# Kernel optimization log

Hardware: AMD Instinct MI355X
Metric: run time of the kernel (lower is better)

## Reference

```python
import jax, jax.numpy as jnp
import numpy as np

N_DRUGS = 4096
W_DIM = 512
N_SUB = 10
N_EDGES = 131072


def setup_inputs() -> dict:
    key = jax.random.key(0)
    k1, k2, k3, k4 = jax.random.split(key, 4)
    z_drug = jax.random.normal(k1, (N_DRUGS, W_DIM), dtype=jnp.float32)
    # glorot-ish init for weights
    global_weight = jax.random.normal(k2, (W_DIM, W_DIM), dtype=jnp.float32) * (2.0 / (2 * W_DIM)) ** 0.5
    local_diag = jax.random.normal(k3, (N_SUB, W_DIM), dtype=jnp.float32) * (2.0 / (W_DIM + 1)) ** 0.5
    batch_edges = jax.random.randint(k4, (2, N_EDGES), 0, N_DRUGS, dtype=jnp.int64)
    return {
        "z_drug": z_drug,
        "global_weight": global_weight,
        "local_diag": local_diag,
        "batch_edges": batch_edges,
        "edge_sub_type_idx": 2,
    }


def reference(z_drug, global_weight, local_diag, batch_edges, edge_sub_type_idx):
    # edge_type == 'drug_drug': z1 = z2 = z_drug
    row_embed = z_drug[batch_edges[0]]            # [B, D]
    col_embed = z_drug[batch_edges[1]]            # [B, D]
    d = local_diag[edge_sub_type_idx]             # [D] diagonal of local weight matrix
    # row @ diag(d) @ W @ diag(d) == ((row * d) @ W) * d
    p = ((row_embed * d) @ global_weight) * d     # [B, D]
    # diagonal(p @ col^T) == rowwise dot product
    score = jnp.sum(p * col_embed, axis=-1)       # [B]
    return jax.nn.sigmoid(score)
```

## Files before the change

### kernel.cpp

```cpp
#include <hip/hip_runtime.h>
#include <cstdint>

#define ND 4096
#define D  512

typedef __bf16 bf16x8 __attribute__((ext_vector_type(8)));
typedef float floatx4 __attribute__((ext_vector_type(4)));
typedef unsigned short ushort8 __attribute__((ext_vector_type(8)));

__device__ __forceinline__ float bf2f(unsigned short b) {
    return __uint_as_float(((unsigned int)b) << 16);
}
__device__ __forceinline__ unsigned short f2bf(float f) {
    unsigned int u = __float_as_uint(f);
    u += 0x7fffu + ((u >> 16) & 1u);
    return (unsigned short)(u >> 16);
}
__device__ __forceinline__ float lo16(unsigned int u) { return __uint_as_float(u << 16); }
__device__ __forceinline__ float hi16(unsigned int u) { return __uint_as_float(u & 0xffff0000u); }

__device__ __forceinline__ void gll16(const void* g, void* l) {
    __builtin_amdgcn_global_load_lds((const __attribute__((address_space(1))) unsigned int*)g,
                                     (__attribute__((address_space(3))) unsigned int*)l,
                                     16, 0, 0);
}

union U8B8 { ushort8 u; bf16x8 b; };

__device__ __forceinline__ int2 detect_flags(const unsigned short* z, const int* ed) {
    int lane = threadIdx.x & 63;
    unsigned short u = z[lane];
    int e = (u >> 7) & 0xFF;
    unsigned long long b0 = __ballot(e >= 96 && e <= 160);
    unsigned long long b1 = __ballot(ed[2 * lane + 1] == 0);
    int2 f;
    f.x = (__popcll(b0) >= 56) ? 1 : 0;
    f.y = (__popcll(b1) >= 56) ? 1 : 0;
    return f;
}

__global__ __launch_bounds__(256) void make_mt(const void* __restrict__ Wv,
                                               const void* __restrict__ ldv,
                                               const int* __restrict__ sub,
                                               unsigned short* __restrict__ Mt,
                                               const unsigned short* __restrict__ zdet,
                                               const int* __restrict__ eddet) {
    __shared__ float lds[64][65];
    int2 f = detect_flags(zdet, eddet);
    int bf = f.x;
    int su = sub[0];
    if ((unsigned)su > 9u) su = 2;
    int k0 = blockIdx.x * 64, n0 = blockIdx.y * 64;
    int j = threadIdx.x & 63;
    int w = threadIdx.x >> 6;

#pragma unroll
    for (int r = 0; r < 16; r++) {
        int k = k0 + w * 16 + r;
        float v = bf ? bf2f(((const unsigned short*)Wv)[k * D + n0 + j])
                     : ((const float*)Wv)[k * D + n0 + j];
        lds[w * 16 + r][j] = v;
    }
    __syncthreads();

    int k = k0 + j;
    float dk = bf ? bf2f(((const unsigned short*)ldv)[su * D + k])
                  : ((const float*)ldv)[su * D + k];
#pragma unroll
    for (int r = 0; r < 16; r++) {
        int n = n0 + w * 16 + r;
        float dn = bf ? bf2f(((const unsigned short*)ldv)[su * D + n])
                      : ((const float*)ldv)[su * D + n];
        Mt[n * D + k] = f2bf(lds[j][w * 16 + r] * dk * dn);
    }
}

template <bool BF>
__device__ void gemm_body(const void* __restrict__ z,
                          const unsigned short* __restrict__ Mt,
                          unsigned short* __restrict__ Y) {
    __shared__ __bf16 As[8 * 512];
    __shared__ __bf16 Bs[8 * 512];
    int tid = threadIdx.x;
    int w = tid >> 6, lane = tid & 63;
    int rl = lane & 15, quad = lane >> 4;
    int tm = blockIdx.x * 64, tn = blockIdx.y * 64;
    int wm = (w >> 1) * 32, wn = (w & 1) * 32;

    floatx4 acc[2][2] = {};
    for (int kk = 0; kk < D; kk += 64) {
        __syncthreads();
#pragma unroll
        for (int t = 0; t < 2; t++) {
            int kb = w * 2 + t;
            gll16(Mt + (tn + lane) * D + kk + kb * 8, Bs + kb * 512);
            if constexpr (BF) {
                gll16((const __bf16*)z + (tm + lane) * D + kk + kb * 8, As + kb * 512);
            } else {
                const float* zf = (const float*)z + (tm + lane) * D + kk + kb * 8;
                float4 f0 = *(const float4*)zf;
                float4 f1 = *(const float4*)(zf + 4);
                U8B8 cv;
                cv.u[0] = f2bf(f0.x); cv.u[1] = f2bf(f0.y); cv.u[2] = f2bf(f0.z); cv.u[3] = f2bf(f0.w);
                cv.u[4] = f2bf(f1.x); cv.u[5] = f2bf(f1.y); cv.u[6] = f2bf(f1.z); cv.u[7] = f2bf(f1.w);
                *(bf16x8*)(As + kb * 512 + lane * 8) = cv.b;
            }
        }
        __syncthreads();
#pragma unroll
        for (int kc = 0; kc < 64; kc += 32) {
            int kb0 = kc >> 3;
            bf16x8 a0 = *(const bf16x8*)(As + (kb0 + quad) * 512 + (wm + rl) * 8);
            bf16x8 a1 = *(const bf16x8*)(As + (kb0 + quad) * 512 + (wm + 16 + rl) * 8);
            bf16x8 b0 = *(const bf16x8*)(Bs + (kb0 + quad) * 512 + (wn + rl) * 8);
            bf16x8 b1 = *(const bf16x8*)(Bs + (kb0 + quad) * 512 + (wn + 16 + rl) * 8);
            acc[0][0] = __builtin_amdgcn_mfma_f32_16x16x32_bf16(a0, b0, acc[0][0], 0, 0, 0);
            acc[0][1] = __builtin_amdgcn_mfma_f32_16x16x32_bf16(a0, b1, acc[0][1], 0, 0, 0);
            acc[1][0] = __builtin_amdgcn_mfma_f32_16x16x32_bf16(a1, b0, acc[1][0], 0, 0, 0);
            acc[1][1] = __builtin_amdgcn_mfma_f32_16x16x32_bf16(a1, b1, acc[1][1], 0, 0, 0);
        }
    }
#pragma unroll
    for (int j = 0; j < 2; j++) {
        int col = tn + wn + j * 16 + rl;
#pragma unroll
        for (int i = 0; i < 2; i++) {
            int rbase = tm + wm + i * 16 + quad * 4;
#pragma unroll
            for (int r = 0; r < 4; r++)
                Y[(rbase + r) * D + col] = f2bf(acc[i][j][r]);
        }
    }
}

__global__ __launch_bounds__(256) void gemm_kernel(const void* __restrict__ z,
                                                   const unsigned short* __restrict__ Mt,
                                                   unsigned short* __restrict__ Y,
                                                   const int* __restrict__ eddet) {
    int2 f = detect_flags((const unsigned short*)z, eddet);
    if (f.x) gemm_body<true>(z, Mt, Y);
    else     gemm_body<false>(z, Mt, Y);
}

template <bool BF, bool I64>
__device__ void edge_body(const unsigned short* __restrict__ Y,
                          const void* __restrict__ z,
                          const int* __restrict__ ed,
                          float* __restrict__ partial,
                          void* __restrict__ out,
                          int E, int pass) {
    int gid = blockIdx.x * 256 + threadIdx.x;
    int lane = threadIdx.x & 63;
    int e = (gid >> 6) * 4 + (lane >> 4);
    int l = lane & 15;
    if (e >= E) return;
    int r, c;
    if constexpr (I64) { r = ed[2 * e]; c = ed[2 * (E + e)]; }
    else               { r = ed[e];     c = ed[E + e]; }
    r &= ND - 1; c &= ND - 1;

    int col = pass * 128 + l * 8;
    uint4 yu = *(const uint4*)(Y + r * D + col);
    float y0 = lo16(yu.x), y1 = hi16(yu.x), y2 = lo16(yu.y), y3 = hi16(yu.y);
    float y4 = lo16(yu.z), y5 = hi16(yu.z), y6 = lo16(yu.w), y7 = hi16(yu.w);
    float s;
    if constexpr (BF) {
        uint4 zu = *(const uint4*)((const unsigned short*)z + c * D + col);
        s  = y0 * lo16(zu.x) + y1 * hi16(zu.x);
        s += y2 * lo16(zu.y) + y3 * hi16(zu.y);
        s += y4 * lo16(zu.z) + y5 * hi16(zu.z);
        s += y6 * lo16(zu.w) + y7 * hi16(zu.w);
    } else {
        const float* zf = (const float*)z + c * D + col;
        float4 f0 = *(const float4*)zf;
        float4 f1 = *(const float4*)(zf + 4);
        s  = y0 * f0.x + y1 * f0.y + y2 * f0.z + y3 * f0.w;
        s += y4 * f1.x + y5 * f1.y + y6 * f1.z + y7 * f1.w;
    }
#pragma unroll
    for (int off = 8; off; off >>= 1)
        s += __shfl_xor(s, off, 64);

    if (l == 0) {
        if (pass == 0)      partial[e] = s;
        else if (pass < 3)  partial[e] += s;
        else {
            float t = s + partial[e];
            if (!(t > -1e30f && t < 1e30f)) t = 0.0f;
            float sig = 1.0f / (1.0f + __expf(-t));
            if constexpr (BF) ((unsigned short*)out)[e] = f2bf(sig);
            else              ((float*)out)[e] = sig;
        }
    }
}

__global__ __launch_bounds__(256) void edge_kernel(const unsigned short* __restrict__ Y,
                                                   const void* __restrict__ z,
                                                   const int* __restrict__ ed,
                                                   float* __restrict__ partial,
                                                   void* __restrict__ out,
                                                   int E, int pass) {
    int2 f = detect_flags((const unsigned short*)z, ed);
    if (f.x) { if (f.y) edge_body<true, true>(Y, z, ed, partial, out, E, pass);
               else     edge_body<true, false>(Y, z, ed, partial, out, E, pass); }
    else     { if (f.y) edge_body<false, true>(Y, z, ed, partial, out, E, pass);
               else     edge_body<false, false>(Y, z, ed, partial, out, E, pass); }
}

extern "C" void kernel_launch(void* const* d_in, const int* in_sizes, int n_in,
                              void* d_out, int out_size, void* d_ws, size_t ws_size,
                              hipStream_t stream) {
    const void* z     = d_in[0];
    const void* W     = d_in[1];
    const void* ldiag = d_in[2];
    const int* edges  = (const int*)d_in[3];
    const int* sub    = (const int*)d_in[4];
    int E = out_size;

    char* ws = (char*)d_ws;
    unsigned short* Y  = (unsigned short*)ws;
    unsigned short* Mt = (unsigned short*)(ws + 4194304);
    float* partial     = (float*)(ws + 4194304 + 524288);

    make_mt<<<dim3(D / 64, D / 64), 256, 0, stream>>>(W, ldiag, sub, Mt,
                                                      (const unsigned short*)z, edges);
    gemm_kernel<<<dim3(ND / 64, D / 64), 256, 0, stream>>>(z, Mt, Y, edges);
    int eblocks = (E + 15) / 16;
    for (int p = 0; p < 4; p++)
        edge_kernel<<<eblocks, 256, 0, stream>>>(Y, z, edges, partial, d_out, E, p);
}
```

Baseline: 126.7 us.

## Fuse all stages into one cooperative persistent kernel with grid syncs

Replaces the six separate launches (transform, GEMM, four edge passes) with a single cooperative kernel of 512 blocks that runs transform, GEMM and two column-half edge passes separated by grid-wide syncs. The edge stage is restructured so each wave loads 64 edge indices once and shuffles them out, processing 256 columns per pass with 32-lane reductions, and keeps partial sums in LDS instead of global memory. This aims to remove launch gaps and redundant index loads, in exchange for grid-sync overhead and a residency requirement. A fallback multi-kernel path is used if the cooperative launch fails.

```diff
diff --git a/kernel.cpp b/kernel.cpp
--- a/kernel.cpp
+++ b/kernel.cpp
@@ -1,8 +1,12 @@
 #include <hip/hip_runtime.h>
+#include <hip/hip_cooperative_groups.h>
 #include <cstdint>
+
+namespace cg = cooperative_groups;
 
 #define ND 4096
 #define D  512
+#define NBLK 512
 
 typedef __bf16 bf16x8 __attribute__((ext_vector_type(8)));
 typedef float floatx4 __attribute__((ext_vector_type(4)));
@@ -39,30 +43,21 @@
     return f;
 }
 
-__global__ __launch_bounds__(256) void make_mt(const void* __restrict__ Wv,
-                                               const void* __restrict__ ldv,
-                                               const int* __restrict__ sub,
-                                               unsigned short* __restrict__ Mt,
-                                               const unsigned short* __restrict__ zdet,
-                                               const int* __restrict__ eddet) {
-    __shared__ float lds[64][65];
-    int2 f = detect_flags(zdet, eddet);
-    int bf = f.x;
+__device__ void make_mt_body(const void* __restrict__ Wv, const void* __restrict__ ldv,
+                             const int* __restrict__ sub, int bf,
+                             unsigned short* __restrict__ Mt, int b, float (*xp)[65]) {
     int su = sub[0];
     if ((unsigned)su > 9u) su = 2;
-    int k0 = blockIdx.x * 64, n0 = blockIdx.y * 64;
-    int j = threadIdx.x & 63;
-    int w = threadIdx.x >> 6;
-
+    int k0 = (b & 7) * 64, n0 = (b >> 3) * 64;
+    int j = threadIdx.x & 63, w = threadIdx.x >> 6;
 #pragma unroll
     for (int r = 0; r < 16; r++) {
         int k = k0 + w * 16 + r;
         float v = bf ? bf2f(((const unsigned short*)Wv)[k * D + n0 + j])
                      : ((const float*)Wv)[k * D + n0 + j];
-        lds[w * 16 + r][j] = v;
+        xp[w * 16 + r][j] = v;
     }
     __syncthreads();
-
     int k = k0 + j;
     float dk = bf ? bf2f(((const unsigned short*)ldv)[su * D + k])
                   : ((const float*)ldv)[su * D + k];
@@ -71,20 +66,18 @@
         int n = n0 + w * 16 + r;
         float dn = bf ? bf2f(((const unsigned short*)ldv)[su * D + n])
                       : ((const float*)ldv)[su * D + n];
-        Mt[n * D + k] = f2bf(lds[j][w * 16 + r] * dk * dn);
+        Mt[n * D + k] = f2bf(xp[j][w * 16 + r] * dk * dn);
     }
 }
 
 template <bool BF>
-__device__ void gemm_body(const void* __restrict__ z,
-                          const unsigned short* __restrict__ Mt,
-                          unsigned short* __restrict__ Y) {
-    __shared__ __bf16 As[8 * 512];
-    __shared__ __bf16 Bs[8 * 512];
+__device__ void gemm_body(const void* __restrict__ z, const unsigned short* __restrict__ Mt,
+                          unsigned short* __restrict__ Y, int b,
+                          __bf16* As, __bf16* Bs) {
     int tid = threadIdx.x;
     int w = tid >> 6, lane = tid & 63;
     int rl = lane & 15, quad = lane >> 4;
-    int tm = blockIdx.x * 64, tn = blockIdx.y * 64;
+    int tm = (b >> 3) * 64, tn = (b & 7) * 64;
     int wm = (w >> 1) * 32, wn = (w & 1) * 32;
 
     floatx4 acc[2][2] = {};
@@ -133,78 +126,122 @@
     }
 }
 
-__global__ __launch_bounds__(256) void gemm_kernel(const void* __restrict__ z,
-                                                   const unsigned short* __restrict__ Mt,
-                                                   unsigned short* __restrict__ Y,
-                                                   const int* __restrict__ eddet) {
+template <bool BF, bool I64>
+__device__ void edge_half(const unsigned short* __restrict__ Y, const void* __restrict__ z,
+                          const int* __restrict__ ed, void* __restrict__ out,
+                          int E, int half, float* pbuf, int pbase) {
+    int lane = threadIdx.x & 63;
+    int w = threadIdx.x >> 6;
+    int wid = blockIdx.x * 4 + w;
+    int base = wid * 64;
+    int le = base + lane;
+    int r_l = 0, c_l = 0;
+    if (le < E) {
+        if constexpr (I64) { r_l = ed[2 * le]; c_l = ed[2 * (E + le)]; }
+        else               { r_l = ed[le];     c_l = ed[E + le]; }
+    }
+    r_l &= ND - 1; c_l &= ND - 1;
+    int g = lane >> 5;
+    int l = lane & 31;
+    int colbase = half * 256 + l * 8;
+
+#pragma unroll 4
+    for (int i = 0; i < 32; i++) {
+        int sube = i * 2 + g;
+        int r = __shfl(r_l, sube, 64);
+        int c = __shfl(c_l, sube, 64);
+        uint4 yu = *(const uint4*)(Y + r * D + colbase);
+        float y0 = lo16(yu.x), y1 = hi16(yu.x), y2 = lo16(yu.y), y3 = hi16(yu.y);
+        float y4 = lo16(yu.z), y5 = hi16(yu.z), y6 = lo16(yu.w), y7 = hi16(yu.w);
+        float s;
+        if constexpr (BF) {
+            uint4 zu = *(const uint4*)((const unsigned short*)z + c * D + colbase);
+            s  = y0 * lo16(zu.x) + y1 * hi16(zu.x);
+            s += y2 * lo16(zu.y) + y3 * hi16(zu.y);
+            s += y4 * lo16(zu.z) + y5 * hi16(zu.z);
+            s += y6 * lo16(zu.w) + y7 * hi16(zu.w);
+        } else {
+            const float* zf = (const float*)z + c * D + colbase;
+            float4 f0 = *(const float4*)zf;
+            float4 f1 = *(const float4*)(zf + 4);
+            s  = y0 * f0.x + y1 * f0.y + y2 * f0.z + y3 * f0.w;
+            s += y4 * f1.x + y5 * f1.y + y6 * f1.z + y7 * f1.w;
+        }
+#pragma unroll
+        for (int off = 16; off; off >>= 1)
+            s += __shfl_xor(s, off, 64);
+
+        if (l == 0 && base + sube < E) {
+            if (half == 0) {
+                pbuf[pbase + sube] = s;
+            } else {
+                float t = s + pbuf[pbase + sube];
+                if (!(t > -1e30f && t < 1e30f)) t = 0.0f;
+                float sig = 1.0f / (1.0f + __expf(-t));
+                if constexpr (BF) ((unsigned short*)out)[base + sube] = f2bf(sig);
+                else              ((float*)out)[base + sube] = sig;
+            }
+        }
+    }
+}
+
+__global__ __launch_bounds__(256, 2) void mega(const void* z, const void* Wv, const void* ldv,
+                                               const int* ed, const int* sub, void* out, int E,
+                                               unsigned short* Mt, unsigned short* Y) {
+    __shared__ float xp[64][65];
+    __shared__ __bf16 As[8 * 512];
+    __shared__ __bf16 Bs[8 * 512];
+    __shared__ float pls[256];
+    cg::grid_group grid = cg::this_grid();
+    int b = blockIdx.x;
+    int2 f = detect_flags((const unsigned short*)z, ed);
+
+    if (b < 64) make_mt_body(Wv, ldv, sub, f.x, Mt, b, xp);
+    __threadfence();
+    grid.sync();
+
+    if (f.x) gemm_body<true>(z, Mt, Y, b, As, Bs);
+    else     gemm_body<false>(z, Mt, Y, b, As, Bs);
+    __threadfence();
+    grid.sync();
+
+    int pbase = (threadIdx.x >> 6) * 64;
+    if (f.x) { if (f.y) edge_half<true, true >(Y, z, ed, out, E, 0, pls, pbase);
+               else     edge_half<true, false>(Y, z, ed, out, E, 0, pls, pbase); }
+    else     { if (f.y) edge_half<false, true >(Y, z, ed, out, E, 0, pls, pbase);
+               else     edge_half<false, false>(Y, z, ed, out, E, 0, pls, pbase); }
+    __threadfence();
+    grid.sync();
+
+    if (f.x) { if (f.y) edge_half<true, true >(Y, z, ed, out, E, 1, pls, pbase);
+               else     edge_half<true, false>(Y, z, ed, out, E, 1, pls, pbase); }
+    else     { if (f.y) edge_half<false, true >(Y, z, ed, out, E, 1, pls, pbase);
+               else     edge_half<false, false>(Y, z, ed, out, E, 1, pls, pbase); }
+}
+
+__global__ __launch_bounds__(256) void fb_make_mt(const void* Wv, const void* ldv,
+                                                  const int* sub, unsigned short* Mt,
+                                                  const unsigned short* zdet, const int* eddet) {
+    __shared__ float xp[64][65];
+    int2 f = detect_flags(zdet, eddet);
+    make_mt_body(Wv, ldv, sub, f.x, Mt, blockIdx.x, xp);
+}
+__global__ __launch_bounds__(256) void fb_gemm(const void* z, const unsigned short* Mt,
+                                               unsigned short* Y, const int* eddet) {
+    __shared__ __bf16 As[8 * 512], Bs[8 * 512];
     int2 f = detect_flags((const unsigned short*)z, eddet);
-    if (f.x) gemm_body<true>(z, Mt, Y);
-    else     gemm_body<false>(z, Mt, Y);
-}
-
-template <bool BF, bool I64>
-__device__ void edge_body(const unsigned short* __restrict__ Y,
-                          const void* __restrict__ z,
-                          const int* __restrict__ ed,
-                          float* __restrict__ partial,
-                          void* __restrict__ out,
-                          int E, int pass) {
-    int gid = blockIdx.x * 256 + threadIdx.x;
-    int lane = threadIdx.x & 63;
-    int e = (gid >> 6) * 4 + (lane >> 4);
-    int l = lane & 15;
-    if (e >= E) return;
-    int r, c;
-    if constexpr (I64) { r = ed[2 * e]; c = ed[2 * (E + e)]; }
-    else               { r = ed[e];     c = ed[E + e]; }
-    r &= ND - 1; c &= ND - 1;
-
-    int col = pass * 128 + l * 8;
-    uint4 yu = *(const uint4*)(Y + r * D + col);
-    float y0 = lo16(yu.x), y1 = hi16(yu.x), y2 = lo16(yu.y), y3 = hi16(yu.y);
-    float y4 = lo16(yu.z), y5 = hi16(yu.z), y6 = lo16(yu.w), y7 = hi16(yu.w);
-    float s;
-    if constexpr (BF) {
-        uint4 zu = *(const uint4*)((const unsigned short*)z + c * D + col);
-        s  = y0 * lo16(zu.x) + y1 * hi16(zu.x);
-        s += y2 * lo16(zu.y) + y3 * hi16(zu.y);
-        s += y4 * lo16(zu.z) + y5 * hi16(zu.z);
-        s += y6 * lo16(zu.w) + y7 * hi16(zu.w);
-    } else {
-        const float* zf = (const float*)z + c * D + col;
-        float4 f0 = *(const float4*)zf;
-        float4 f1 = *(const float4*)(zf + 4);
-        s  = y0 * f0.x + y1 * f0.y + y2 * f0.z + y3 * f0.w;
-        s += y4 * f1.x + y5 * f1.y + y6 * f1.z + y7 * f1.w;
-    }
-#pragma unroll
-    for (int off = 8; off; off >>= 1)
-        s += __shfl_xor(s, off, 64);
-
-    if (l == 0) {
-        if (pass == 0)      partial[e] = s;
-        else if (pass < 3)  partial[e] += s;
-        else {
-            float t = s + partial[e];
-            if (!(t > -1e30f && t < 1e30f)) t = 0.0f;
-            float sig = 1.0f / (1.0f + __expf(-t));
-            if constexpr (BF) ((unsigned short*)out)[e] = f2bf(sig);
-            else              ((float*)out)[e] = sig;
-        }
-    }
-}
-
-__global__ __launch_bounds__(256) void edge_kernel(const unsigned short* __restrict__ Y,
-                                                   const void* __restrict__ z,
-                                                   const int* __restrict__ ed,
-                                                   float* __restrict__ partial,
-                                                   void* __restrict__ out,
-                                                   int E, int pass) {
+    if (f.x) gemm_body<true>(z, Mt, Y, blockIdx.x, As, Bs);
+    else     gemm_body<false>(z, Mt, Y, blockIdx.x, As, Bs);
+}
+__global__ __launch_bounds__(256) void fb_edge(const unsigned short* Y, const void* z,
+                                               const int* ed, float* partial, void* out,
+                                               int E, int half) {
     int2 f = detect_flags((const unsigned short*)z, ed);
-    if (f.x) { if (f.y) edge_body<true, true>(Y, z, ed, partial, out, E, pass);
-               else     edge_body<true, false>(Y, z, ed, partial, out, E, pass); }
-    else     { if (f.y) edge_body<false, true>(Y, z, ed, partial, out, E, pass);
-               else     edge_body<false, false>(Y, z, ed, partial, out, E, pass); }
+    int pbase = (blockIdx.x * 4 + (threadIdx.x >> 6)) * 64;
+    if (f.x) { if (f.y) edge_half<true, true >(Y, z, ed, out, E, half, partial, pbase);
+               else     edge_half<true, false>(Y, z, ed, out, E, half, partial, pbase); }
+    else     { if (f.y) edge_half<false, true >(Y, z, ed, out, E, half, partial, pbase);
+               else     edge_half<false, false>(Y, z, ed, out, E, half, partial, pbase); }
 }
 
 extern "C" void kernel_launch(void* const* d_in, const int* in_sizes, int n_in,
@@ -222,10 +259,14 @@
     unsigned short* Mt = (unsigned short*)(ws + 4194304);
     float* partial     = (float*)(ws + 4194304 + 524288);
 
-    make_mt<<<dim3(D / 64, D / 64), 256, 0, stream>>>(W, ldiag, sub, Mt,
-                                                      (const unsigned short*)z, edges);
-    gemm_kernel<<<dim3(ND / 64, D / 64), 256, 0, stream>>>(z, Mt, Y, edges);
-    int eblocks = (E + 15) / 16;
-    for (int p = 0; p < 4; p++)
-        edge_kernel<<<eblocks, 256, 0, stream>>>(Y, z, edges, partial, d_out, E, p);
-}
+    void* kargs[] = { (void*)&z, (void*)&W, (void*)&ldiag, (void*)&edges, (void*)&sub,
+                      (void*)&d_out, (void*)&E, (void*)&Mt, (void*)&Y };
+    hipError_t err = hipLaunchCooperativeKernel((const void*)mega, dim3(NBLK), dim3(256),
+                                                kargs, 0, stream);
+    if (err != hipSuccess) {
+        fb_make_mt<<<64, 256, 0, stream>>>(W, ldiag, sub, Mt, (const unsigned short*)z, edges);
+        fb_gemm<<<NBLK, 256, 0, stream>>>(z, Mt, Y, edges);
+        fb_edge<<<NBLK, 256, 0, stream>>>(Y, z, edges, partial, d_out, E, 0);
+        fb_edge<<<NBLK, 256, 0, stream>>>(Y, z, edges, partial, d_out, E, 1);
+    }
+}
```

After: 423.8 us. 235% more time.

## Fuse four edge-score passes into one kernel with per-wave edge batching

Applied to the files above, without the earlier changes.

Replaces four column-slice edge passes, which kept partial sums in a workspace buffer, with a single edge kernel. Each wave loads 32 edge indices once, broadcasts them by shuffle, and accumulates the full 512-wide dot products in registers before reducing and applying the sigmoid. This removes three launches and the partial read/write traffic. The make_mt and gemm grids also become 1D with remapped tile order, which changes block scheduling and L2 locality. The cost is higher register use (16 accumulators per lane) and less parallelism per launch.

```diff
diff --git a/kernel.cpp b/kernel.cpp
--- a/kernel.cpp
+++ b/kernel.cpp
@@ -45,24 +45,21 @@
                                                unsigned short* __restrict__ Mt,
                                                const unsigned short* __restrict__ zdet,
                                                const int* __restrict__ eddet) {
-    __shared__ float lds[64][65];
+    __shared__ float xp[64][65];
     int2 f = detect_flags(zdet, eddet);
     int bf = f.x;
     int su = sub[0];
     if ((unsigned)su > 9u) su = 2;
-    int k0 = blockIdx.x * 64, n0 = blockIdx.y * 64;
-    int j = threadIdx.x & 63;
-    int w = threadIdx.x >> 6;
-
+    int k0 = (blockIdx.x & 7) * 64, n0 = (blockIdx.x >> 3) * 64;
+    int j = threadIdx.x & 63, w = threadIdx.x >> 6;
 #pragma unroll
     for (int r = 0; r < 16; r++) {
         int k = k0 + w * 16 + r;
         float v = bf ? bf2f(((const unsigned short*)Wv)[k * D + n0 + j])
                      : ((const float*)Wv)[k * D + n0 + j];
-        lds[w * 16 + r][j] = v;
+        xp[w * 16 + r][j] = v;
     }
     __syncthreads();
-
     int k = k0 + j;
     float dk = bf ? bf2f(((const unsigned short*)ldv)[su * D + k])
                   : ((const float*)ldv)[su * D + k];
@@ -71,20 +68,19 @@
         int n = n0 + w * 16 + r;
         float dn = bf ? bf2f(((const unsigned short*)ldv)[su * D + n])
                       : ((const float*)ldv)[su * D + n];
-        Mt[n * D + k] = f2bf(lds[j][w * 16 + r] * dk * dn);
+        Mt[n * D + k] = f2bf(xp[j][w * 16 + r] * dk * dn);
     }
 }
 
 template <bool BF>
-__device__ void gemm_body(const void* __restrict__ z,
-                          const unsigned short* __restrict__ Mt,
+__device__ void gemm_body(const void* __restrict__ z, const unsigned short* __restrict__ Mt,
                           unsigned short* __restrict__ Y) {
     __shared__ __bf16 As[8 * 512];
     __shared__ __bf16 Bs[8 * 512];
     int tid = threadIdx.x;
     int w = tid >> 6, lane = tid & 63;
     int rl = lane & 15, quad = lane >> 4;
-    int tm = blockIdx.x * 64, tn = blockIdx.y * 64;
+    int tm = (blockIdx.x >> 3) * 64, tn = (blockIdx.x & 7) * 64;
     int wm = (w >> 1) * 32, wn = (w & 1) * 32;
 
     floatx4 acc[2][2] = {};
@@ -143,51 +139,64 @@
 }
 
 template <bool BF, bool I64>
-__device__ void edge_body(const unsigned short* __restrict__ Y,
-                          const void* __restrict__ z,
-                          const int* __restrict__ ed,
-                          float* __restrict__ partial,
-                          void* __restrict__ out,
-                          int E, int pass) {
-    int gid = blockIdx.x * 256 + threadIdx.x;
+__device__ void edge_body(const unsigned short* __restrict__ Y, const void* __restrict__ z,
+                          const int* __restrict__ ed, void* __restrict__ out, int E) {
     int lane = threadIdx.x & 63;
-    int e = (gid >> 6) * 4 + (lane >> 4);
-    int l = lane & 15;
-    if (e >= E) return;
-    int r, c;
-    if constexpr (I64) { r = ed[2 * e]; c = ed[2 * (E + e)]; }
-    else               { r = ed[e];     c = ed[E + e]; }
-    r &= ND - 1; c &= ND - 1;
-
-    int col = pass * 128 + l * 8;
-    uint4 yu = *(const uint4*)(Y + r * D + col);
-    float y0 = lo16(yu.x), y1 = hi16(yu.x), y2 = lo16(yu.y), y3 = hi16(yu.y);
-    float y4 = lo16(yu.z), y5 = hi16(yu.z), y6 = lo16(yu.w), y7 = hi16(yu.w);
-    float s;
-    if constexpr (BF) {
-        uint4 zu = *(const uint4*)((const unsigned short*)z + c * D + col);
-        s  = y0 * lo16(zu.x) + y1 * hi16(zu.x);
-        s += y2 * lo16(zu.y) + y3 * hi16(zu.y);
-        s += y4 * lo16(zu.z) + y5 * hi16(zu.z);
-        s += y6 * lo16(zu.w) + y7 * hi16(zu.w);
-    } else {
-        const float* zf = (const float*)z + c * D + col;
-        float4 f0 = *(const float4*)zf;
-        float4 f1 = *(const float4*)(zf + 4);
-        s  = y0 * f0.x + y1 * f0.y + y2 * f0.z + y3 * f0.w;
-        s += y4 * f1.x + y5 * f1.y + y6 * f1.z + y7 * f1.w;
-    }
-#pragma unroll
-    for (int off = 8; off; off >>= 1)
-        s += __shfl_xor(s, off, 64);
-
-    if (l == 0) {
-        if (pass == 0)      partial[e] = s;
-        else if (pass < 3)  partial[e] += s;
-        else {
-            float t = s + partial[e];
-            if (!(t > -1e30f && t < 1e30f)) t = 0.0f;
-            float sig = 1.0f / (1.0f + __expf(-t));
+    int w = threadIdx.x >> 6;
+    int base = (blockIdx.x * 4 + w) * 32;
+    int li = base + (lane & 31);
+    int r_l = 0, c_l = 0;
+    if (li < E) {
+        if constexpr (I64) { r_l = ed[2 * li]; c_l = ed[2 * (E + li)]; }
+        else               { r_l = ed[li];     c_l = ed[E + li]; }
+    }
+    r_l &= ND - 1; c_l &= ND - 1;
+    int g = lane >> 5;
+    int l = lane & 31;
+
+    float ps[16];
+#pragma unroll
+    for (int i = 0; i < 16; i++) ps[i] = 0.f;
+
+#pragma unroll
+    for (int half = 0; half < 2; half++) {
+        int colbase = half * 256 + l * 8;
+#pragma unroll
+        for (int i = 0; i < 16; i++) {
+            int sube = i * 2 + g;
+            int r = __shfl(r_l, sube, 64);
+            int c = __shfl(c_l, sube, 64);
+            uint4 yu = *(const uint4*)(Y + r * D + colbase);
+            float s;
+            if constexpr (BF) {
+                uint4 zu = *(const uint4*)((const unsigned short*)z + c * D + colbase);
+                s  = lo16(yu.x) * lo16(zu.x) + hi16(yu.x) * hi16(zu.x);
+                s += lo16(yu.y) * lo16(zu.y) + hi16(yu.y) * hi16(zu.y);
+                s += lo16(yu.z) * lo16(zu.z) + hi16(yu.z) * hi16(zu.z);
+                s += lo16(yu.w) * lo16(zu.w) + hi16(yu.w) * hi16(zu.w);
+            } else {
+                const float* zf = (const float*)z + c * D + colbase;
+                float4 f0 = *(const float4*)zf;
+                float4 f1 = *(const float4*)(zf + 4);
+                s  = lo16(yu.x) * f0.x + hi16(yu.x) * f0.y;
+                s += lo16(yu.y) * f0.z + hi16(yu.y) * f0.w;
+                s += lo16(yu.z) * f1.x + hi16(yu.z) * f1.y;
+                s += lo16(yu.w) * f1.z + hi16(yu.w) * f1.w;
+            }
+            ps[i] += s;
+        }
+    }
+
+#pragma unroll
+    for (int i = 0; i < 16; i++) {
+        float s = ps[i];
+#pragma unroll
+        for (int off = 16; off; off >>= 1)
+            s += __shfl_xor(s, off, 64);
+        int e = base + i * 2 + g;
+        if (l == 0 && e < E) {
+            if (!(s > -1e30f && s < 1e30f)) s = 0.0f;
+            float sig = 1.0f / (1.0f + __expf(-s));
             if constexpr (BF) ((unsigned short*)out)[e] = f2bf(sig);
             else              ((float*)out)[e] = sig;
         }
@@ -197,14 +206,12 @@
 __global__ __launch_bounds__(256) void edge_kernel(const unsigned short* __restrict__ Y,
                                                    const void* __restrict__ z,
                                                    const int* __restrict__ ed,
-                                                   float* __restrict__ partial,
-                                                   void* __restrict__ out,
-                                                   int E, int pass) {
+                                                   void* __restrict__ out, int E) {
     int2 f = detect_flags((const unsigned short*)z, ed);
-    if (f.x) { if (f.y) edge_body<true, true>(Y, z, ed, partial, out, E, pass);
-               else     edge_body<true, false>(Y, z, ed, partial, out, E, pass); }
-    else     { if (f.y) edge_body<false, true>(Y, z, ed, partial, out, E, pass);
-               else     edge_body<false, false>(Y, z, ed, partial, out, E, pass); }
+    if (f.x) { if (f.y) edge_body<true, true >(Y, z, ed, out, E);
+               else     edge_body<true, false>(Y, z, ed, out, E); }
+    else     { if (f.y) edge_body<false, true >(Y, z, ed, out, E);
+               else     edge_body<false, false>(Y, z, ed, out, E); }
 }
 
 extern "C" void kernel_launch(void* const* d_in, const int* in_sizes, int n_in,
@@ -220,12 +227,9 @@
     char* ws = (char*)d_ws;
     unsigned short* Y  = (unsigned short*)ws;
     unsigned short* Mt = (unsigned short*)(ws + 4194304);
-    float* partial     = (float*)(ws + 4194304 + 524288);
-
-    make_mt<<<dim3(D / 64, D / 64), 256, 0, stream>>>(W, ldiag, sub, Mt,
-                                                      (const unsigned short*)z, edges);
-    gemm_kernel<<<dim3(ND / 64, D / 64), 256, 0, stream>>>(z, Mt, Y, edges);
-    int eblocks = (E + 15) / 16;
-    for (int p = 0; p < 4; p++)
-        edge_kernel<<<eblocks, 256, 0, stream>>>(Y, z, edges, partial, d_out, E, p);
-}
+
+    make_mt<<<64, 256, 0, stream>>>(W, ldiag, sub, Mt, (const unsigned short*)z, edges);
+    gemm_kernel<<<512, 256, 0, stream>>>(z, Mt, Y, edges);
+    int eblocks = (E + 127) / 128;
+    edge_kernel<<<eblocks, 256, 0, stream>>>(Y, z, edges, d_out, E);
+}
```

Result: slower. 140.4 us (+10.8%).
